# Kernel tuning notes

Hardware: AMD Instinct MI355X
Metric: run time of the kernel (lower is better)

## Reference

```python
import jax, jax.numpy as jnp
import numpy as np

B, C, T, E = 8, 64, 128, 256
TYPE_NUM, NF = 40, 128
KS = (5, 4, 3)
NEG = -1e10


def setup_inputs() -> dict:
    key = jax.random.key(0)
    ks = jax.random.split(key, 10)
    s = 0.02
    return {
        "query": jax.random.normal(ks[0], (C, E), jnp.float32),
        "context": jax.random.normal(ks[1], (B, T, E), jnp.float32),
        "mask": jax.random.randint(ks[2], (B, T), 0, 2, jnp.int32),
        "W_hidden": jax.random.normal(ks[3], (4 * E, 4 * E), jnp.float32) * s,
        "b_hidden": jnp.zeros((4 * E,), jnp.float32),
        "W_v": jax.random.normal(ks[4], (1, 4 * E), jnp.float32) * s,
        "b_v": jnp.zeros((1,), jnp.float32),
        "W_lin": jax.random.normal(ks[5], (E, 4 * E), jnp.float32) * s,
        "b_lin": jnp.zeros((E,), jnp.float32),
        "conv_w0": jax.random.normal(ks[6], (NF, E, KS[0]), jnp.float32) * s,
        "conv_b0": jnp.zeros((NF,), jnp.float32),
        "conv_w1": jax.random.normal(ks[7], (NF, E, KS[1]), jnp.float32) * s,
        "conv_b1": jnp.zeros((NF,), jnp.float32),
        "conv_w2": jax.random.normal(ks[8], (NF, E, KS[2]), jnp.float32) * s,
        "conv_b2": jnp.zeros((NF,), jnp.float32),
        "W_cnn": jax.random.normal(ks[9], (TYPE_NUM, NF * 3), jnp.float32) * s,
        "b_cnn": jnp.zeros((TYPE_NUM,), jnp.float32),
    }


def _pair_feat(a, b):
    # [.., e] x2 -> [.., 4e]: [a, b, |a-b|, a*b]
    return jnp.concatenate([a, b, jnp.abs(a - b), a * b], axis=-1)


def _conv1d(x, w, b):
    # x: [b, e, c], w: [f, e, k] (torch Conv1d layout) -> [b, f, c-k+1]
    y = jax.lax.conv_general_dilated(
        x, w, window_strides=(1,), padding="VALID",
        dimension_numbers=("NCH", "OIH", "NCH"))
    return y + b[None, :, None]


def reference(query, context, mask, W_hidden, b_hidden, W_v, b_v,
              W_lin, b_lin, conv_w0, conv_b0, conv_w1, conv_b1,
              conv_w2, conv_b2, W_cnn, b_cnn):
    b, t, e = context.shape
    c = query.shape[0]
    q_ = jnp.broadcast_to(query[None, :, None, :], (b, c, t, e))
    ctx_ = jnp.broadcast_to(context[:, None, :, :], (b, c, t, e))
    feat = _pair_feat(q_, ctx_)                                 # [b,c,t,4e]
    h = jnp.tanh(feat @ W_hidden.T + b_hidden)                  # [b,c,t,4e]
    scores = (h @ W_v.T + b_v)[..., 0]                          # [b,c,t]
    scores = jnp.where((mask < 1)[:, None, :], NEG, scores)
    attn = jax.nn.softmax(scores, axis=-1)                      # [b,c,t]
    g = jnp.einsum("bct,bte->bce", attn, context)               # [b,c,e]
    q2 = jnp.broadcast_to(query[None], (b, c, e))
    h2 = jnp.tanh(_pair_feat(q2, g) @ W_hidden.T + b_hidden)    # [b,c,4e]
    x = h2 @ W_lin.T + b_lin                                    # [b,c,e]
    xT = jnp.transpose(x, (0, 2, 1))                            # [b,e,c]
    pooled = []
    for w, bb in ((conv_w0, conv_b0), (conv_w1, conv_b1), (conv_w2, conv_b2)):
        y = jax.nn.relu(_conv1d(xT, w, bb))                     # [b,f,c-k+1]
        pooled.append(jnp.max(y, axis=2))                       # [b,f]
    cnn = jnp.concatenate(pooled, axis=1)                       # [b,3f]
    return cnn @ W_cnn.T + b_cnn                                # [b,type_num]
```

## Files before the change

### kernel.cpp

```cpp
#include <hip/hip_runtime.h>
#include <math.h>


typedef __bf16 bf16x8 __attribute__((ext_vector_type(8)));
typedef float  f32x4  __attribute__((ext_vector_type(4)));

__device__ __forceinline__ float ftanh(float v) {
    float t = __expf(2.f * v);
    return 1.f - 2.f * __builtin_amdgcn_rcpf(t + 1.f);
}

__device__ __forceinline__ void gld_lds16(const __bf16* g, __bf16* l) {
    __builtin_amdgcn_global_load_lds(
        (const __attribute__((address_space(1))) void*)g,
        (__attribute__((address_space(3))) void*)l, 16, 0, 0);
}

__global__ __launch_bounds__(256) void gemm_tn_kernel(
    const float* __restrict__ A, int lda,
    const float* __restrict__ B, int ldb,
    const float* __restrict__ bias,
    float* __restrict__ C, int ldc, int K)
{
    __shared__ float As[16][68];
    __shared__ float Bs[16][68];
    const int tid = threadIdx.x;
    const int m0 = blockIdx.y * 64, n0 = blockIdx.x * 64;
    const int tm = tid >> 4, tn = tid & 15;
    const int lr = tid >> 2;
    const int lc = (tid & 3) * 4;

    float acc[4][4];
#pragma unroll
    for (int i = 0; i < 4; ++i)
#pragma unroll
        for (int j = 0; j < 4; ++j) acc[i][j] = 0.f;

    for (int k0 = 0; k0 < K; k0 += 16) {
        float4 av = *reinterpret_cast<const float4*>(A + (size_t)(m0 + lr) * lda + k0 + lc);
        float4 bv = *reinterpret_cast<const float4*>(B + (size_t)(n0 + lr) * ldb + k0 + lc);
        As[lc + 0][lr] = av.x; As[lc + 1][lr] = av.y; As[lc + 2][lr] = av.z; As[lc + 3][lr] = av.w;
        Bs[lc + 0][lr] = bv.x; Bs[lc + 1][lr] = bv.y; Bs[lc + 2][lr] = bv.z; Bs[lc + 3][lr] = bv.w;
        __syncthreads();
#pragma unroll
        for (int kk = 0; kk < 16; ++kk) {
            float4 a = *reinterpret_cast<const float4*>(&As[kk][tm * 4]);
            float4 b = *reinterpret_cast<const float4*>(&Bs[kk][tn * 4]);
            float ar[4] = {a.x, a.y, a.z, a.w};
            float br[4] = {b.x, b.y, b.z, b.w};
#pragma unroll
            for (int i = 0; i < 4; ++i)
#pragma unroll
                for (int j = 0; j < 4; ++j) acc[i][j] += ar[i] * br[j];
        }
        __syncthreads();
    }

#pragma unroll
    for (int i = 0; i < 4; ++i) {
        int m = m0 + tm * 4 + i;
        float vals[4];
#pragma unroll
        for (int j = 0; j < 4; ++j) {
            int n = n0 + tn * 4 + j;
            vals[j] = acc[i][j] + (bias ? bias[n] : 0.f);
        }
        float4 o; o.x = vals[0]; o.y = vals[1]; o.z = vals[2]; o.w = vals[3];
        *reinterpret_cast<float4*>(C + (size_t)m * ldc + n0 + tn * 4) = o;
    }
}

__global__ void cvt_kernel(const float* __restrict__ Wh, const float* __restrict__ Wl,
                           const float* __restrict__ ctx,
                           const float* __restrict__ cw0, const float* __restrict__ cw1,
                           const float* __restrict__ cw2,
                           __bf16* __restrict__ Whbf, __bf16* __restrict__ Whbf_t,
                           __bf16* __restrict__ Wlbf, __bf16* __restrict__ ctxbf,
                           float* __restrict__ wt0, float* __restrict__ wt1,
                           float* __restrict__ wt2, float* __restrict__ gsc)
{
    int idx = blockIdx.x * 256 + threadIdx.x;
    if (idx < 1048576) { Whbf[idx] = (__bf16)Wh[idx]; return; }
    if (idx < 1114112) {
        int di = idx - 1048576;
        int ng = di >> 13, kc = (di >> 10) & 7;
        int row = (di >> 3) & 127, kgp = di & 7;
        int kg = kgp ^ (row & 7);
        const float* s = Wh + (size_t)(ng * 128 + row) * 1024 + 512 + kc * 64 + kg * 8;
        bf16x8 u;
#pragma unroll
        for (int i = 0; i < 8; ++i) u[i] = (__bf16)s[i];
        *reinterpret_cast<bf16x8*>(Whbf_t + (size_t)di * 8) = u;
        return;
    }
    if (idx < 1376256) { int j = idx - 1114112; Wlbf[j] = (__bf16)Wl[j]; return; }
    if (idx < 1409024) {
        int di = idx - 1376256;
        const float* s = ctx + (size_t)di * 8;
        bf16x8 u;
#pragma unroll
        for (int i = 0; i < 8; ++i) u[i] = (__bf16)s[i];
        *reinterpret_cast<bf16x8*>(ctxbf + (size_t)di * 8) = u;
        return;
    }
    if (idx < 1572864) {
        int j = idx - 1409024; int f = j & 127, rest = j >> 7;
        int i = rest % 5, e = rest / 5;
        wt0[j] = cw0[(size_t)(f * 256 + e) * 5 + i]; return;
    }
    if (idx < 1703936) {
        int j = idx - 1572864; int f = j & 127, rest = j >> 7;
        int i = rest & 3, e = rest >> 2;
        wt1[j] = cw1[(size_t)(f * 256 + e) * 4 + i]; return;
    }
    if (idx < 1802240) {
        int j = idx - 1703936; int f = j & 127, rest = j >> 7;
        int i = rest % 3, e = rest / 3;
        wt2[j] = cw2[(size_t)(f * 256 + e) * 3 + i]; return;
    }
    gsc[idx - 1802240] = 0.f;
}

__global__ __launch_bounds__(512, 4) void attn_mfma_kernel(
    const float* __restrict__ q,
    const float* __restrict__ ctx,
    const __bf16* __restrict__ Whbf_t,
    const float* __restrict__ Wv,
    const float* __restrict__ Apre,
    const float* __restrict__ Bpre,
    float* __restrict__ gsc)
{
    __shared__ __bf16 Us[256 * 64];
    __shared__ __bf16 Ws[128 * 64];
    __shared__ float qc[512];
    __shared__ float sc[256];

    const int tid = threadIdx.x;
    const int cpair = blockIdx.x >> 3, ng = blockIdx.x & 7;
    const int b = cpair >> 5, c0 = (cpair & 31) * 2;
    const int wave = tid >> 6, lane = tid & 63;
    const int w1 = wave & 1, w0 = wave >> 1;
    const int m0 = w0 * 64;
    const int l15 = lane & 15, quad = lane >> 4;
    const int swz = l15 & 7;
    const int kg = tid & 7;

    qc[tid] = q[(size_t)(c0 + (tid >> 8)) * 256 + (tid & 255)];
    if (tid < 256) sc[tid] = 0.f;
    __syncthreads();

    f32x4 acc[4][4];
#pragma unroll
    for (int mi = 0; mi < 4; ++mi)
#pragma unroll
        for (int ni = 0; ni < 4; ++ni) acc[mi][ni] = (f32x4){0.f, 0.f, 0.f, 0.f};

    for (int kc = 0; kc < 8; ++kc) {
        const bool isabs = (kc < 4);
        const int e0 = (kc & 3) * 64;
        const int eb = e0 + kg * 8;
        float qA[8], qB[8];
#pragma unroll
        for (int i = 0; i < 8; ++i) { qA[i] = qc[eb + i]; qB[i] = qc[256 + eb + i]; }
        bf16x8 u0[2], u1[2];
#pragma unroll
        for (int it = 0; it < 2; ++it) {
            const int trow = it * 64 + (tid >> 3);
            const float* cp = ctx + (size_t)(b * 128 + trow) * 256 + eb;
            float4 cl0 = *reinterpret_cast<const float4*>(cp);
            float4 cl1 = *reinterpret_cast<const float4*>(cp + 4);
            float cv[8] = {cl0.x, cl0.y, cl0.z, cl0.w, cl1.x, cl1.y, cl1.z, cl1.w};
#pragma unroll
            for (int i = 0; i < 8; ++i) {
                u0[it][i] = (__bf16)(isabs ? fabsf(qA[i] - cv[i]) : qA[i] * cv[i]);
                u1[it][i] = (__bf16)(isabs ? fabsf(qB[i] - cv[i]) : qB[i] * cv[i]);
            }
        }
        __syncthreads();
        const __bf16* wtile = Whbf_t + (size_t)(ng * 8 + kc) * 8192;
#pragma unroll
        for (int it = 0; it < 2; ++it) {
            int gidx = wave * 128 + it * 64;
            gld_lds16(wtile + (size_t)(gidx + lane) * 8, &Ws[gidx * 8]);
        }
#pragma unroll
        for (int it = 0; it < 2; ++it) {
            const int trow = it * 64 + (tid >> 3);
            const int off = (kg ^ (trow & 7)) * 8;
            *reinterpret_cast<bf16x8*>(&Us[trow * 64 + off]) = u0[it];
            *reinterpret_cast<bf16x8*>(&Us[(trow + 128) * 64 + off]) = u1[it];
        }
        __syncthreads();
#pragma unroll
        for (int ks = 0; ks < 2; ++ks) {
            const int c8 = (((ks * 4 + quad) ^ swz)) * 8;
            bf16x8 a[4], bfr[4];
#pragma unroll
            for (int mi = 0; mi < 4; ++mi)
                a[mi] = *reinterpret_cast<const bf16x8*>(
                    &Us[(m0 + mi * 16 + l15) * 64 + c8]);
#pragma unroll
            for (int ni = 0; ni < 4; ++ni)
                bfr[ni] = *reinterpret_cast<const bf16x8*>(
                    &Ws[(w1 * 64 + ni * 16 + l15) * 64 + c8]);
#pragma unroll
            for (int mi = 0; mi < 4; ++mi)
#pragma unroll
                for (int ni = 0; ni < 4; ++ni)
                    acc[mi][ni] = __builtin_amdgcn_mfma_f32_16x16x32_bf16(
                        a[mi], bfr[ni], acc[mi][ni], 0, 0, 0);
        }
    }

    const int jcol = ng * 128 + w1 * 64 + l15;
    const int c = c0 + (w0 >> 1);
    float av[4], wv[4];
#pragma unroll
    for (int ni = 0; ni < 4; ++ni) {
        av[ni] = Apre[(size_t)c * 1024 + jcol + ni * 16];
        wv[ni] = Wv[jcol + ni * 16];
    }
#pragma unroll
    for (int mi = 0; mi < 4; ++mi) {
        const int tb = (w0 & 1) * 64 + mi * 16 + quad * 4;
        float p[4];
#pragma unroll
        for (int r = 0; r < 4; ++r) {
            const float* bp = Bpre + (size_t)(b * 128 + tb + r) * 1024 + jcol;
            float s = 0.f;
#pragma unroll
            for (int ni = 0; ni < 4; ++ni)
                s += ftanh(acc[mi][ni][r] + av[ni] + bp[ni * 16]) * wv[ni];
            p[r] = s;
        }
#pragma unroll
        for (int off = 1; off < 16; off <<= 1)
#pragma unroll
            for (int r = 0; r < 4; ++r) p[r] += __shfl_xor(p[r], off, 16);
        if (l15 == 0) {
#pragma unroll
            for (int r = 0; r < 4; ++r)
                atomicAdd(&sc[(w0 >> 1) * 128 + tb + r], p[r]);
        }
    }
    __syncthreads();

    if (tid < 256) atomicAdd(&gsc[(size_t)(b * 64 + c0) * 128 + tid], sc[tid]);
}

__global__ __launch_bounds__(256) void attn_tail_kernel(
    const float* __restrict__ ctx, const int* __restrict__ mask,
    const float* __restrict__ bv, const float* __restrict__ gsc,
    float* __restrict__ g)
{
    __shared__ float sc[128];
    __shared__ float red;
    const int tid = threadIdx.x;
    const int bc = blockIdx.x, b = bc >> 6;

    if (tid < 128) {
        float s = gsc[(size_t)bc * 128 + tid] + bv[0];
        if (mask[b * 128 + tid] < 1) s = -1e10f;
        sc[tid] = s;
    }
    __syncthreads();
    if (tid < 64) {
        float m = fmaxf(sc[tid], sc[tid + 64]);
        for (int off = 32; off; off >>= 1) m = fmaxf(m, __shfl_xor(m, off, 64));
        if (tid == 0) red = m;
    }
    __syncthreads();
    const float mx = red;
    if (tid < 128) sc[tid] = __expf(sc[tid] - mx);
    __syncthreads();
    if (tid < 64) {
        float s = sc[tid] + sc[tid + 64];
        for (int off = 32; off; off >>= 1) s += __shfl_xor(s, off, 64);
        if (tid == 0) red = s;
    }
    __syncthreads();
    const float inv = 1.f / red;

    float gv = 0.f;
    for (int t = 0; t < 128; ++t) gv += sc[t] * ctx[(size_t)(b * 128 + t) * 256 + tid];
    g[(size_t)bc * 256 + tid] = gv * inv;
}

__global__ void feat2_kernel(const float* __restrict__ q, const float* __restrict__ g,
                             __bf16* __restrict__ feat2)
{
    int row = blockIdx.x, e = threadIdx.x;
    int c = row & 63;
    float qv = q[c * 256 + e], gv = g[row * 256 + e];
    __bf16* o = feat2 + (size_t)row * 768 + e;
    o[0]   = (__bf16)gv;
    o[256] = (__bf16)fabsf(qv - gv);
    o[512] = (__bf16)(qv * gv);
}

template <int ACT, int OUTBF, int BMODE>
__global__ __launch_bounds__(256) void mfma_gemm_kernel(
    const __bf16* __restrict__ A, int lda,
    const __bf16* __restrict__ B, int ldb,
    const float* __restrict__ bias, void* __restrict__ Cout,
    int K, int ldc)
{
    __shared__ __bf16 As[64 * 72];
    __shared__ __bf16 Bs[64 * 72];
    const int tid = threadIdx.x;
    const int wave = tid >> 6, lane = tid & 63;
    const int w0 = wave >> 1, w1 = wave & 1;
    const int l15 = lane & 15, quad = lane >> 4;
    const int m0 = blockIdx.y * 64, n0 = blockIdx.x * 64;

    f32x4 acc[2][2];
#pragma unroll
    for (int mi = 0; mi < 2; ++mi)
#pragma unroll
        for (int ni = 0; ni < 2; ++ni) acc[mi][ni] = (f32x4){0.f, 0.f, 0.f, 0.f};

    for (int k0 = 0; k0 < K; k0 += 64) {
        __syncthreads();
#pragma unroll
        for (int it = 0; it < 2; ++it) {
            int idx = tid + it * 256;
            int row = idx >> 3, kgi = idx & 7;
            int4 va = *reinterpret_cast<const int4*>(A + (size_t)(m0 + row) * lda + k0 + kgi * 8);
            *reinterpret_cast<int4*>(&As[row * 72 + kgi * 8]) = va;
            int4 vb = *reinterpret_cast<const int4*>(B + (size_t)(n0 + row) * ldb + k0 + kgi * 8);
            *reinterpret_cast<int4*>(&Bs[row * 72 + kgi * 8]) = vb;
        }
        __syncthreads();
#pragma unroll
        for (int ks = 0; ks < 2; ++ks) {
            bf16x8 a[2], bb[2];
#pragma unroll
            for (int mi = 0; mi < 2; ++mi)
                a[mi] = *reinterpret_cast<const bf16x8*>(
                    &As[(w0 * 32 + mi * 16 + l15) * 72 + ks * 32 + quad * 8]);
#pragma unroll
            for (int ni = 0; ni < 2; ++ni)
                bb[ni] = *reinterpret_cast<const bf16x8*>(
                    &Bs[(w1 * 32 + ni * 16 + l15) * 72 + ks * 32 + quad * 8]);
#pragma unroll
            for (int mi = 0; mi < 2; ++mi)
#pragma unroll
                for (int ni = 0; ni < 2; ++ni)
                    acc[mi][ni] = __builtin_amdgcn_mfma_f32_16x16x32_bf16(
                        a[mi], bb[ni], acc[mi][ni], 0, 0, 0);
        }
    }

#pragma unroll
    for (int mi = 0; mi < 2; ++mi)
#pragma unroll
        for (int ni = 0; ni < 2; ++ni) {
            int col = n0 + w1 * 32 + ni * 16 + l15;
#pragma unroll
            for (int r = 0; r < 4; ++r) {
                int row = m0 + w0 * 32 + mi * 16 + quad * 4 + r;
                float bsv = (BMODE == 0) ? bias[col]
                          : (BMODE == 1) ? bias[(row & 63) * 1024 + col] : 0.f;
                float v = acc[mi][ni][r] + bsv;
                if (ACT) v = ftanh(v);
                if (OUTBF) ((__bf16*)Cout)[(size_t)row * ldc + col] = (__bf16)v;
                else       ((float*)Cout)[(size_t)row * ldc + col] = v;
            }
        }
}

template <int KW>
__device__ __forceinline__ void conv_body(
    const float* __restrict__ x, const float* __restrict__ wt,
    float* __restrict__ part, int b, int chunk, int bi, float* xs)
{
    const int tid = threadIdx.x;
    const int f = tid & 127, esub = tid >> 7;
    const int e0 = chunk * 64;

#pragma unroll
    for (int it = 0; it < 16; ++it) {
        int idx = tid + it * 256;
        int e = idx & 63, p = idx >> 6;
        xs[e * 72 + p] = x[(size_t)(b * 64 + p) * 256 + e0 + e];
    }
    __syncthreads();

    float acc[64];
#pragma unroll
    for (int p = 0; p < 64; ++p) acc[p] = 0.f;

    for (int ei = 0; ei < 32; ++ei) {
        const int eL = esub * 32 + ei;
        float wreg[KW];
#pragma unroll
        for (int i = 0; i < KW; ++i)
            wreg[i] = wt[(size_t)((e0 + eL) * KW + i) * 128 + f];
        float xv[68];
#pragma unroll
        for (int k4 = 0; k4 < 17; ++k4) {
            float4 v = *reinterpret_cast<const float4*>(&xs[eL * 72 + k4 * 4]);
            xv[k4 * 4 + 0] = v.x; xv[k4 * 4 + 1] = v.y;
            xv[k4 * 4 + 2] = v.z; xv[k4 * 4 + 3] = v.w;
        }
#pragma unroll
        for (int i = 0; i < KW; ++i)
#pragma unroll
            for (int p = 0; p < 64; ++p)
                acc[p] = fmaf(wreg[i], xv[p + i], acc[p]);
    }

    float* op = part + ((size_t)(bi * 2 + esub)) * 8192 + f;
#pragma unroll
    for (int p = 0; p < 64; ++p) op[p * 128] = acc[p];
}

__global__ __launch_bounds__(256) void conv_partial_kernel(
    const float* __restrict__ x,
    const float* __restrict__ wt0, const float* __restrict__ wt1,
    const float* __restrict__ wt2, float* __restrict__ part)
{
    __shared__ float xs[64 * 72];
    const int bi = blockIdx.x;
    const int kw = bi >> 5, b = (bi >> 2) & 7, chunk = bi & 3;
    if (kw == 0)      conv_body<5>(x, wt0, part, b, chunk, bi, xs);
    else if (kw == 1) conv_body<4>(x, wt1, part, b, chunk, bi, xs);
    else              conv_body<3>(x, wt2, part, b, chunk, bi, xs);
}

__global__ __launch_bounds__(128) void reduce_pool_kernel(
    const float* __restrict__ part,
    const float* __restrict__ b0, const float* __restrict__ b1,
    const float* __restrict__ b2, float* __restrict__ cnn)
{
    const int bi = blockIdx.x;
    const int kw = bi >> 3, b = bi & 7;
    const int f = threadIdx.x;
    const int KW = 5 - kw, P = 64 - KW + 1;
    const float bias = (kw == 0 ? b0 : kw == 1 ? b1 : b2)[f];
    float mx = 0.f;
    for (int p = 0; p < P; ++p) {
        float s = 0.f;
#pragma unroll
        for (int c4 = 0; c4 < 4; ++c4)
#pragma unroll
            for (int es = 0; es < 2; ++es)
                s += part[((size_t)((kw * 32 + b * 4 + c4) * 2 + es)) * 8192 + p * 128 + f];
        s += bias;
        mx = fmaxf(mx, s);
    }
    cnn[b * 384 + kw * 128 + f] = mx;
}

__global__ void final_kernel(const float* __restrict__ cnn, const float* __restrict__ Wc,
                             const float* __restrict__ bc, float* __restrict__ out)
{
    int o = threadIdx.x;
    if (o >= 320) return;
    int b = o / 40, t = o - b * 40;
    float s = bc[t];
    for (int i = 0; i < 384; ++i) s += cnn[b * 384 + i] * Wc[t * 384 + i];
    out[o] = s;
}

extern "C" void kernel_launch(void* const* d_in, const int* in_sizes, int n_in,
                              void* d_out, int out_size, void* d_ws, size_t ws_size,
                              hipStream_t stream)
{
    (void)in_sizes; (void)n_in; (void)out_size; (void)ws_size;
    const float* q    = (const float*)d_in[0];
    const float* ctx  = (const float*)d_in[1];
    const int*   mask = (const int*)d_in[2];
    const float* Wh   = (const float*)d_in[3];
    const float* bh   = (const float*)d_in[4];
    const float* Wv   = (const float*)d_in[5];
    const float* bv   = (const float*)d_in[6];
    const float* Wl   = (const float*)d_in[7];
    const float* bl   = (const float*)d_in[8];
    const float* cw0  = (const float*)d_in[9];
    const float* cb0  = (const float*)d_in[10];
    const float* cw1  = (const float*)d_in[11];
    const float* cb1  = (const float*)d_in[12];
    const float* cw2  = (const float*)d_in[13];
    const float* cb2  = (const float*)d_in[14];
    const float* Wc   = (const float*)d_in[15];
    const float* bc   = (const float*)d_in[16];

    float* ws   = (float*)d_ws;
    float* Apre = ws;
    float* g    = Apre + 65536;
    float* x    = g + 131072;
    float* cnn  = x + 131072;
    float* part = cnn + 3072;
    float* wt0  = part + 1572864;
    float* wt1  = wt0 + 163840;
    float* wt2  = wt1 + 131072;
    __bf16* bfb    = (__bf16*)(wt2 + 98304);
    __bf16* Whbf   = bfb;
    __bf16* Wlbf   = bfb + 1048576;
    __bf16* feat2b = bfb + 1310720;
    __bf16* h2b    = bfb + 1703936;
    float*  gsc    = (float*)(bfb + 2228224);
    __bf16* Whbf_t = (__bf16*)part;
    __bf16* ctxbf  = Whbf_t + 524288;
    float*  Bpre   = (float*)(ctxbf + 262144);

    dim3 blk(256);
    cvt_kernel<<<7296, blk, 0, stream>>>(Wh, Wl, ctx, cw0, cw1, cw2,
                                         Whbf, Whbf_t, Wlbf, ctxbf, wt0, wt1, wt2, gsc);
    gemm_tn_kernel<<<dim3(16, 1), blk, 0, stream>>>(q, 256, Wh, 1024, bh, Apre, 1024, 256);
    mfma_gemm_kernel<0, 0, 2><<<dim3(16, 16), blk, 0, stream>>>(
        ctxbf, 256, Whbf + 256, 1024, nullptr, Bpre, 256, 1024);
    attn_mfma_kernel<<<2048, dim3(512), 0, stream>>>(q, ctx, Whbf_t, Wv, Apre, Bpre, gsc);
    attn_tail_kernel<<<512, blk, 0, stream>>>(ctx, mask, bv, gsc, g);
    feat2_kernel<<<512, blk, 0, stream>>>(q, g, feat2b);
    mfma_gemm_kernel<1, 1, 1><<<dim3(16, 8), blk, 0, stream>>>(
        feat2b, 768, Whbf + 256, 1024, Apre, h2b, 768, 1024);
    mfma_gemm_kernel<0, 0, 0><<<dim3(4, 8), blk, 0, stream>>>(
        h2b, 1024, Wlbf, 1024, bl, x, 1024, 256);
    conv_partial_kernel<<<96, blk, 0, stream>>>(x, wt0, wt1, wt2, part);
    reduce_pool_kernel<<<24, 128, 0, stream>>>(part, cb0, cb1, cb2, cnn);
    final_kernel<<<1, 320, 0, stream>>>(cnn, Wc, bc, (float*)d_out);
}
```

Measured before the change: 321.0 us.

## Vectorize conversion, fuse feat2 into attention tail, split conv and pool work

```diff
diff --git a/kernel.cpp b/kernel.cpp
--- a/kernel.cpp
+++ b/kernel.cpp
@@ -77,48 +77,77 @@
                            __bf16* __restrict__ Whbf, __bf16* __restrict__ Whbf_t,
                            __bf16* __restrict__ Wlbf, __bf16* __restrict__ ctxbf,
                            float* __restrict__ wt0, float* __restrict__ wt1,
-                           float* __restrict__ wt2, float* __restrict__ gsc)
+                           float* __restrict__ wt2, float* __restrict__ gsc,
+                           float* __restrict__ cnn)
 {
     int idx = blockIdx.x * 256 + threadIdx.x;
-    if (idx < 1048576) { Whbf[idx] = (__bf16)Wh[idx]; return; }
-    if (idx < 1114112) {
-        int di = idx - 1048576;
+    if (idx < 131072) {
+        const float* s = Wh + (size_t)idx * 8;
+        float4 f0 = *reinterpret_cast<const float4*>(s);
+        float4 f1 = *reinterpret_cast<const float4*>(s + 4);
+        bf16x8 u;
+        u[0] = (__bf16)f0.x; u[1] = (__bf16)f0.y; u[2] = (__bf16)f0.z; u[3] = (__bf16)f0.w;
+        u[4] = (__bf16)f1.x; u[5] = (__bf16)f1.y; u[6] = (__bf16)f1.z; u[7] = (__bf16)f1.w;
+        *reinterpret_cast<bf16x8*>(Whbf + (size_t)idx * 8) = u;
+        return;
+    }
+    if (idx < 196608) {
+        int di = idx - 131072;
         int ng = di >> 13, kc = (di >> 10) & 7;
         int row = (di >> 3) & 127, kgp = di & 7;
         int kg = kgp ^ (row & 7);
         const float* s = Wh + (size_t)(ng * 128 + row) * 1024 + 512 + kc * 64 + kg * 8;
+        float4 f0 = *reinterpret_cast<const float4*>(s);
+        float4 f1 = *reinterpret_cast<const float4*>(s + 4);
         bf16x8 u;
-#pragma unroll
-        for (int i = 0; i < 8; ++i) u[i] = (__bf16)s[i];
+        u[0] = (__bf16)f0.x; u[1] = (__bf16)f0.y; u[2] = (__bf16)f0.z; u[3] = (__bf16)f0.w;
+        u[4] = (__bf16)f1.x; u[5] = (__bf16)f1.y; u[6] = (__bf16)f1.z; u[7] = (__bf16)f1.w;
         *reinterpret_cast<bf16x8*>(Whbf_t + (size_t)di * 8) = u;
         return;
     }
-    if (idx < 1376256) { int j = idx - 1114112; Wlbf[j] = (__bf16)Wl[j]; return; }
-    if (idx < 1409024) {
-        int di = idx - 1376256;
+    if (idx < 229376) {
+        int di = idx - 196608;
+        const float* s = Wl + (size_t)di * 8;
+        float4 f0 = *reinterpret_cast<const float4*>(s);
+        float4 f1 = *reinterpret_cast<const float4*>(s + 4);
+        bf16x8 u;
+        u[0] = (__bf16)f0.x; u[1] = (__bf16)f0.y; u[2] = (__bf16)f0.z; u[3] = (__bf16)f0.w;
+        u[4] = (__bf16)f1.x; u[5] = (__bf16)f1.y; u[6] = (__bf16)f1.z; u[7] = (__bf16)f1.w;
+        *reinterpret_cast<bf16x8*>(Wlbf + (size_t)di * 8) = u;
+        return;
+    }
+    if (idx < 262144) {
+        int di = idx - 229376;
         const float* s = ctx + (size_t)di * 8;
+        float4 f0 = *reinterpret_cast<const float4*>(s);
+        float4 f1 = *reinterpret_cast<const float4*>(s + 4);
         bf16x8 u;
-#pragma unroll
-        for (int i = 0; i < 8; ++i) u[i] = (__bf16)s[i];
+        u[0] = (__bf16)f0.x; u[1] = (__bf16)f0.y; u[2] = (__bf16)f0.z; u[3] = (__bf16)f0.w;
+        u[4] = (__bf16)f1.x; u[5] = (__bf16)f1.y; u[6] = (__bf16)f1.z; u[7] = (__bf16)f1.w;
         *reinterpret_cast<bf16x8*>(ctxbf + (size_t)di * 8) = u;
         return;
     }
-    if (idx < 1572864) {
-        int j = idx - 1409024; int f = j & 127, rest = j >> 7;
+    if (idx < 425984) {
+        int j = idx - 262144; int f = j & 127, rest = j >> 7;
         int i = rest % 5, e = rest / 5;
         wt0[j] = cw0[(size_t)(f * 256 + e) * 5 + i]; return;
     }
-    if (idx < 1703936) {
-        int j = idx - 1572864; int f = j & 127, rest = j >> 7;
+    if (idx < 557056) {
+        int j = idx - 425984; int f = j & 127, rest = j >> 7;
         int i = rest & 3, e = rest >> 2;
         wt1[j] = cw1[(size_t)(f * 256 + e) * 4 + i]; return;
     }
-    if (idx < 1802240) {
-        int j = idx - 1703936; int f = j & 127, rest = j >> 7;
+    if (idx < 655360) {
+        int j = idx - 557056; int f = j & 127, rest = j >> 7;
         int i = rest % 3, e = rest / 3;
         wt2[j] = cw2[(size_t)(f * 256 + e) * 3 + i]; return;
     }
-    gsc[idx - 1802240] = 0.f;
+    if (idx < 671744) {
+        int di = idx - 655360;
+        reinterpret_cast<float4*>(gsc)[di] = (float4){0.f, 0.f, 0.f, 0.f};
+        return;
+    }
+    if (idx < 674816) cnn[idx - 671744] = 0.f;
 }
 
 __global__ __launch_bounds__(512, 4) void attn_mfma_kernel(
@@ -251,12 +280,12 @@
 __global__ __launch_bounds__(256) void attn_tail_kernel(
     const float* __restrict__ ctx, const int* __restrict__ mask,
     const float* __restrict__ bv, const float* __restrict__ gsc,
-    float* __restrict__ g)
+    const float* __restrict__ q, __bf16* __restrict__ feat2)
 {
     __shared__ float sc[128];
     __shared__ float red;
     const int tid = threadIdx.x;
-    const int bc = blockIdx.x, b = bc >> 6;
+    const int bc = blockIdx.x, b = bc >> 6, c = bc & 63;
 
     if (tid < 128) {
         float s = gsc[(size_t)bc * 128 + tid] + bv[0];
@@ -283,16 +312,9 @@
 
     float gv = 0.f;
     for (int t = 0; t < 128; ++t) gv += sc[t] * ctx[(size_t)(b * 128 + t) * 256 + tid];
-    g[(size_t)bc * 256 + tid] = gv * inv;
-}
-
-__global__ void feat2_kernel(const float* __restrict__ q, const float* __restrict__ g,
-                             __bf16* __restrict__ feat2)
-{
-    int row = blockIdx.x, e = threadIdx.x;
-    int c = row & 63;
-    float qv = q[c * 256 + e], gv = g[row * 256 + e];
-    __bf16* o = feat2 + (size_t)row * 768 + e;
+    gv *= inv;
+    const float qv = q[(size_t)c * 256 + tid];
+    __bf16* o = feat2 + (size_t)bc * 768 + tid;
     o[0]   = (__bf16)gv;
     o[256] = (__bf16)fabsf(qv - gv);
     o[512] = (__bf16)(qv * gv);
@@ -372,7 +394,7 @@
 template <int KW>
 __device__ __forceinline__ void conv_body(
     const float* __restrict__ x, const float* __restrict__ wt,
-    float* __restrict__ part, int b, int chunk, int bi, float* xs)
+    float* __restrict__ part, int b, int chunk, int bi_part, int pbase, float* xs)
 {
     const int tid = threadIdx.x;
     const int f = tid & 127, esub = tid >> 7;
@@ -386,9 +408,9 @@
     }
     __syncthreads();
 
-    float acc[64];
-#pragma unroll
-    for (int p = 0; p < 64; ++p) acc[p] = 0.f;
+    float acc[32];
+#pragma unroll
+    for (int p = 0; p < 32; ++p) acc[p] = 0.f;
 
     for (int ei = 0; ei < 32; ++ei) {
         const int eL = esub * 32 + ei;
@@ -396,23 +418,23 @@
 #pragma unroll
         for (int i = 0; i < KW; ++i)
             wreg[i] = wt[(size_t)((e0 + eL) * KW + i) * 128 + f];
-        float xv[68];
-#pragma unroll
-        for (int k4 = 0; k4 < 17; ++k4) {
-            float4 v = *reinterpret_cast<const float4*>(&xs[eL * 72 + k4 * 4]);
+        float xv[36];
+#pragma unroll
+        for (int k4 = 0; k4 < 9; ++k4) {
+            float4 v = *reinterpret_cast<const float4*>(&xs[eL * 72 + pbase + k4 * 4]);
             xv[k4 * 4 + 0] = v.x; xv[k4 * 4 + 1] = v.y;
             xv[k4 * 4 + 2] = v.z; xv[k4 * 4 + 3] = v.w;
         }
 #pragma unroll
         for (int i = 0; i < KW; ++i)
 #pragma unroll
-            for (int p = 0; p < 64; ++p)
+            for (int p = 0; p < 32; ++p)
                 acc[p] = fmaf(wreg[i], xv[p + i], acc[p]);
     }
 
-    float* op = part + ((size_t)(bi * 2 + esub)) * 8192 + f;
-#pragma unroll
-    for (int p = 0; p < 64; ++p) op[p * 128] = acc[p];
+    float* op = part + ((size_t)(bi_part * 2 + esub)) * 8192 + f;
+#pragma unroll
+    for (int p = 0; p < 32; ++p) op[(pbase + p) * 128] = acc[p];
 }
 
 __global__ __launch_bounds__(256) void conv_partial_kernel(
@@ -422,10 +444,12 @@
 {
     __shared__ float xs[64 * 72];
     const int bi = blockIdx.x;
-    const int kw = bi >> 5, b = (bi >> 2) & 7, chunk = bi & 3;
-    if (kw == 0)      conv_body<5>(x, wt0, part, b, chunk, bi, xs);
-    else if (kw == 1) conv_body<4>(x, wt1, part, b, chunk, bi, xs);
-    else              conv_body<3>(x, wt2, part, b, chunk, bi, xs);
+    const int kw = bi >> 6, b = (bi >> 3) & 7, chunk = (bi >> 1) & 3;
+    const int pbase = (bi & 1) * 32;
+    const int bi_part = kw * 32 + b * 4 + chunk;
+    if (kw == 0)      conv_body<5>(x, wt0, part, b, chunk, bi_part, pbase, xs);
+    else if (kw == 1) conv_body<4>(x, wt1, part, b, chunk, bi_part, pbase, xs);
+    else              conv_body<3>(x, wt2, part, b, chunk, bi_part, pbase, xs);
 }
 
 __global__ __launch_bounds__(128) void reduce_pool_kernel(
@@ -434,22 +458,27 @@
     const float* __restrict__ b2, float* __restrict__ cnn)
 {
     const int bi = blockIdx.x;
-    const int kw = bi >> 3, b = bi & 7;
+    const int kw = bi >> 6, b = (bi >> 3) & 7, pc = bi & 7;
     const int f = threadIdx.x;
     const int KW = 5 - kw, P = 64 - KW + 1;
     const float bias = (kw == 0 ? b0 : kw == 1 ? b1 : b2)[f];
     float mx = 0.f;
-    for (int p = 0; p < P; ++p) {
-        float s = 0.f;
-#pragma unroll
-        for (int c4 = 0; c4 < 4; ++c4)
-#pragma unroll
-            for (int es = 0; es < 2; ++es)
-                s += part[((size_t)((kw * 32 + b * 4 + c4) * 2 + es)) * 8192 + p * 128 + f];
-        s += bias;
-        mx = fmaxf(mx, s);
-    }
-    cnn[b * 384 + kw * 128 + f] = mx;
+#pragma unroll
+    for (int pl = 0; pl < 8; ++pl) {
+        int p = pc * 8 + pl;
+        if (p < P) {
+            float s = 0.f;
+#pragma unroll
+            for (int c4 = 0; c4 < 4; ++c4)
+#pragma unroll
+                for (int es = 0; es < 2; ++es)
+                    s += part[((size_t)((kw * 32 + b * 4 + c4) * 2 + es)) * 8192 + p * 128 + f];
+            s += bias;
+            mx = fmaxf(mx, s);
+        }
+    }
+    if (mx > 0.f)
+        atomicMax((int*)(cnn + b * 384 + kw * 128 + f), __float_as_int(mx));
 }
 
 __global__ void final_kernel(const float* __restrict__ cnn, const float* __restrict__ Wc,
@@ -506,19 +535,19 @@
     float*  Bpre   = (float*)(ctxbf + 262144);
 
     dim3 blk(256);
-    cvt_kernel<<<7296, blk, 0, stream>>>(Wh, Wl, ctx, cw0, cw1, cw2,
-                                         Whbf, Whbf_t, Wlbf, ctxbf, wt0, wt1, wt2, gsc);
+    cvt_kernel<<<2636, blk, 0, stream>>>(Wh, Wl, ctx, cw0, cw1, cw2,
+                                         Whbf, Whbf_t, Wlbf, ctxbf, wt0, wt1, wt2,
+                                         gsc, cnn);
     gemm_tn_kernel<<<dim3(16, 1), blk, 0, stream>>>(q, 256, Wh, 1024, bh, Apre, 1024, 256);
     mfma_gemm_kernel<0, 0, 2><<<dim3(16, 16), blk, 0, stream>>>(
         ctxbf, 256, Whbf + 256, 1024, nullptr, Bpre, 256, 1024);
     attn_mfma_kernel<<<2048, dim3(512), 0, stream>>>(q, ctx, Whbf_t, Wv, Apre, Bpre, gsc);
-    attn_tail_kernel<<<512, blk, 0, stream>>>(ctx, mask, bv, gsc, g);
-    feat2_kernel<<<512, blk, 0, stream>>>(q, g, feat2b);
+    attn_tail_kernel<<<512, blk, 0, stream>>>(ctx, mask, bv, gsc, q, feat2b);
     mfma_gemm_kernel<1, 1, 1><<<dim3(16, 8), blk, 0, stream>>>(
         feat2b, 768, Whbf + 256, 1024, Apre, h2b, 768, 1024);
     mfma_gemm_kernel<0, 0, 0><<<dim3(4, 8), blk, 0, stream>>>(
         h2b, 1024, Wlbf, 1024, bl, x, 1024, 256);
-    conv_partial_kernel<<<96, blk, 0, stream>>>(x, wt0, wt1, wt2, part);
-    reduce_pool_kernel<<<24, 128, 0, stream>>>(part, cb0, cb1, cb2, cnn);
+    conv_partial_kernel<<<192, blk, 0, stream>>>(x, wt0, wt1, wt2, part);
+    reduce_pool_kernel<<<192, dim3(128), 0, stream>>>(part, cb0, cb1, cb2, cnn);
     final_kernel<<<1, 320, 0, stream>>>(cnn, Wc, bc, (float*)d_out);
 }
```

New measurement: 299.9 us. -6.6%, faster.
